# Optimization experiments

Hardware: AMD Instinct MI355X
Metric: run time of the kernel (lower is better)

Reference implementation:

```python
import jax, jax.numpy as jnp
import numpy as np

TOKEN_NUM = 81   # init default token_num
KNN_K = 2        # hardcoded in apply_clustering
LAYER_INDEX = 3


def setup_inputs() -> dict:
    key = jax.random.key(0)
    k1, k2, k3 = jax.random.split(key, 3)
    B, F, N, C = 8, 1024, 17, 512
    x = jax.random.normal(k1, (B, F, N, C), dtype=jnp.float32)
    # nn.Parameter init normal_(std=0.02)
    pos_embed_token = 0.02 * jax.random.normal(k2, (1, TOKEN_NUM, C), dtype=jnp.float32)
    # deterministic stand-in for torch.rand tie-breaker noise on density
    density_noise = jax.random.uniform(k3, (B, F), dtype=jnp.float32)
    return {"x": x, "pos_embed_token": pos_embed_token,
            "density_noise": density_noise, "current_layer": LAYER_INDEX}


def _dpc_knn_index(x_knn, density_noise, cluster_num, k):
    # x_knn: (B, F, C) pooled features; returns sorted cluster-center indices (B, cluster_num)
    B, F, C = x_knn.shape
    sq = jnp.sum(x_knn * x_knn, axis=-1)                       # (B, F)
    d2 = sq[:, :, None] + sq[:, None, :] - 2.0 * jnp.einsum('bic,bjc->bij', x_knn, x_knn)
    dist = jnp.sqrt(jnp.maximum(d2, 0.0)) / jnp.sqrt(jnp.asarray(C, x_knn.dtype))  # cdist / C**0.5
    # k smallest distances (self included, dist 0)
    neg_nearest, _ = jax.lax.top_k(-dist, k)                   # (B, F, k)
    dist_nearest = -neg_nearest
    density = jnp.exp(-jnp.mean(dist_nearest ** 2, axis=-1))   # (B, F)
    density = density + density_noise * 1e-6                   # tie-breaker
    # mask[b,i,j] = density[b,j] > density[b,i]
    mask = (density[:, None, :] > density[:, :, None]).astype(x_knn.dtype)
    dist_max = jnp.max(dist.reshape(B, -1), axis=-1)[:, None, None]
    min_dist = jnp.min(dist * mask + dist_max * (1.0 - mask), axis=-1)  # (B, F)
    score = min_dist * density
    _, index_down = jax.lax.top_k(score, cluster_num)          # (B, cluster_num)
    return jnp.sort(index_down, axis=-1)


def reference(x, pos_embed_token, density_noise, current_layer):
    # forward path only hits clustering when current_layer == layer_index
    if current_layer != LAYER_INDEX:
        return x
    B, F, N, C = x.shape
    # AdaptiveAvgPool1d(1) over joint axis after 'b f n c -> b (f c) n' == mean over n
    x_knn = jnp.mean(x, axis=2)                                # (B, F, C)
    index = _dpc_knn_index(x_knn, density_noise, TOKEN_NUM, KNN_K)
    index = jax.lax.stop_gradient(index)                       # clustering is under no_grad
    # gather selected frames: x[batch, index] -> (B, token_num, N, C)
    compressed = jnp.take_along_axis(x, index[:, :, None, None], axis=1)
    # '+ pos_embed_token' applied per (b n) f c  ==  broadcast over joints
    compressed = compressed + pos_embed_token[:, :, None, :]
    return compressed
```

## Files before the change

kernel.cpp:

```cpp
#include <hip/hip_runtime.h>
#include <math.h>
#include <float.h>

#define BB 8
#define FF 1024
#define NJ 17
#define CH 512
#define TOK 81
#define RCP_SQRT_C 0.04419417382415922f
#define LP 133

typedef short bf16x8 __attribute__((ext_vector_type(8)));
typedef float f32x16 __attribute__((ext_vector_type(16)));

static __device__ inline unsigned short f2bf(float f) {
    __bf16 h = (__bf16)f;
    return __builtin_bit_cast(unsigned short, h);
}
static __device__ inline float bf2f(unsigned short u) {
    return (float)__builtin_bit_cast(__bf16, u);
}


__global__ __launch_bounds__(256) void pool_kernel(const float* __restrict__ x,
                                                   uint4* __restrict__ fhi,
                                                   uint4* __restrict__ flo,
                                                   float* __restrict__ sq) {
    const int t = threadIdx.x;
    const int wid = t >> 6, lane = t & 63;
    const int row0 = blockIdx.x * 4;
    const int row = row0 + wid;
    const int b = row >> 10, f0 = row0 & 1023;
    const float* px = x + (size_t)row * NJ * CH + lane * 8;
    float a[8] = {};
    #pragma unroll
    for (int n = 0; n < NJ; ++n) {
        const float4 v0 = *(const float4*)(px + (size_t)n * CH);
        const float4 v1 = *(const float4*)(px + (size_t)n * CH + 4);
        a[0] += v0.x; a[1] += v0.y; a[2] += v0.z; a[3] += v0.w;
        a[4] += v1.x; a[5] += v1.y; a[6] += v1.z; a[7] += v1.w;
    }
    float ssq = 0.f;
    unsigned short hi[8], lo[8];
    #pragma unroll
    for (int j = 0; j < 8; ++j) {
        const float m = a[j] / 17.0f;
        ssq += m * m;
        hi[j] = f2bf(m);
        lo[j] = f2bf(m - bf2f(hi[j]));
    }
    #pragma unroll
    for (int off = 32; off > 0; off >>= 1) ssq += __shfl_down(ssq, off);
    if (lane == 0) sq[row] = ssq;

    uint4 uh, ul;
    uh.x = (unsigned)hi[0] | ((unsigned)hi[1] << 16);
    uh.y = (unsigned)hi[2] | ((unsigned)hi[3] << 16);
    uh.z = (unsigned)hi[4] | ((unsigned)hi[5] << 16);
    uh.w = (unsigned)hi[6] | ((unsigned)hi[7] << 16);
    ul.x = (unsigned)lo[0] | ((unsigned)lo[1] << 16);
    ul.y = (unsigned)lo[2] | ((unsigned)lo[3] << 16);
    ul.z = (unsigned)lo[4] | ((unsigned)lo[5] << 16);
    ul.w = (unsigned)lo[6] | ((unsigned)lo[7] << 16);
    __shared__ uint4 sh_hi[256], sh_lo[256];
    sh_hi[lane * 4 + wid] = uh;
    sh_lo[lane * 4 + wid] = ul;
    __syncthreads();
    const int k8 = t >> 2, fpr = t & 3;
    const int s = k8 >> 1, h = k8 & 1;
    const size_t o = (((size_t)b * 32 + s) * 2 + h) * 1024 + f0 + fpr;
    fhi[o] = sh_hi[t];
    flo[o] = sh_lo[t];
}

__global__ __launch_bounds__(256) void dist_kernel(const uint4* __restrict__ fhi,
                                                   const uint4* __restrict__ flo,
                                                   const float* __restrict__ sq,
                                                   float* __restrict__ dist) {
    int tri = blockIdx.x, rt = 0;
    while (tri >= 8 - rt) { tri -= 8 - rt; ++rt; }
    const int ct = rt + tri;
    const bool diag = (rt == ct);
    const int b = blockIdx.z;
    const int tid = threadIdx.x;
    const int w = tid >> 6, lane = tid & 63;
    const int R = rt * 128 + (w & 1) * 64;
    const int C = ct * 128 + (w >> 1) * 64;
    const int h = lane >> 5, fr = lane & 31;

    size_t a0 = ((size_t)b * 64 + h) * 1024 + R + fr;
    size_t b0 = ((size_t)b * 64 + h) * 1024 + C + fr;

    f32x16 acc00, acc01, acc10, acc11;
    #pragma unroll
    for (int i = 0; i < 16; ++i) { acc00[i] = 0.f; acc01[i] = 0.f; acc10[i] = 0.f; acc11[i] = 0.f; }

    bf16x8 A0h = *(const bf16x8*)(fhi + a0), A1h = *(const bf16x8*)(fhi + a0 + 32);
    bf16x8 A0l = *(const bf16x8*)(flo + a0), A1l = *(const bf16x8*)(flo + a0 + 32);
    bf16x8 B0h = *(const bf16x8*)(fhi + b0), B1h = *(const bf16x8*)(fhi + b0 + 32);
    bf16x8 B0l = *(const bf16x8*)(flo + b0), B1l = *(const bf16x8*)(flo + b0 + 32);

    #pragma unroll 4
    for (int s = 0; s < 32; ++s) {
        const bf16x8 cA0h = A0h, cA1h = A1h, cA0l = A0l, cA1l = A1l;
        const bf16x8 cB0h = B0h, cB1h = B1h, cB0l = B0l, cB1l = B1l;
        if (s < 31) {
            a0 += 2048; b0 += 2048;
            A0h = *(const bf16x8*)(fhi + a0); A1h = *(const bf16x8*)(fhi + a0 + 32);
            A0l = *(const bf16x8*)(flo + a0); A1l = *(const bf16x8*)(flo + a0 + 32);
            B0h = *(const bf16x8*)(fhi + b0); B1h = *(const bf16x8*)(fhi + b0 + 32);
            B0l = *(const bf16x8*)(flo + b0); B1l = *(const bf16x8*)(flo + b0 + 32);
        }
        acc00 = __builtin_amdgcn_mfma_f32_32x32x16_bf16(cA0h, cB0h, acc00, 0, 0, 0);
        acc01 = __builtin_amdgcn_mfma_f32_32x32x16_bf16(cA0h, cB1h, acc01, 0, 0, 0);
        acc10 = __builtin_amdgcn_mfma_f32_32x32x16_bf16(cA1h, cB0h, acc10, 0, 0, 0);
        acc11 = __builtin_amdgcn_mfma_f32_32x32x16_bf16(cA1h, cB1h, acc11, 0, 0, 0);
        acc00 = __builtin_amdgcn_mfma_f32_32x32x16_bf16(cA0h, cB0l, acc00, 0, 0, 0);
        acc01 = __builtin_amdgcn_mfma_f32_32x32x16_bf16(cA0h, cB1l, acc01, 0, 0, 0);
        acc10 = __builtin_amdgcn_mfma_f32_32x32x16_bf16(cA1h, cB0l, acc10, 0, 0, 0);
        acc11 = __builtin_amdgcn_mfma_f32_32x32x16_bf16(cA1h, cB1l, acc11, 0, 0, 0);
        acc00 = __builtin_amdgcn_mfma_f32_32x32x16_bf16(cA0l, cB0h, acc00, 0, 0, 0);
        acc01 = __builtin_amdgcn_mfma_f32_32x32x16_bf16(cA0l, cB1h, acc01, 0, 0, 0);
        acc10 = __builtin_amdgcn_mfma_f32_32x32x16_bf16(cA1l, cB0h, acc10, 0, 0, 0);
        acc11 = __builtin_amdgcn_mfma_f32_32x32x16_bf16(cA1l, cB1h, acc11, 0, 0, 0);
    }

    __shared__ float lds[64 * LP];
    const int bF = b * FF;
    const int R0 = rt * 128, C0 = ct * 128;
    const float sqc0 = sq[bF + C + fr], sqc1 = sq[bF + C + fr + 32];
    const int lcb = (w >> 1) * 64 + fr;

    #pragma unroll
    for (int p = 0; p < 2; ++p) {
        if ((w & 1) == p) {
            #pragma unroll
            for (int reg = 0; reg < 16; ++reg) {
                const int rp = 4 * h + (reg & 3) + 8 * (reg >> 2);
                const float sqr0 = sq[bF + R + rp];
                const float sqr1 = sq[bF + R + rp + 32];
                lds[rp * LP + lcb] =
                    sqrtf(fmaxf(sqr0 + sqc0 - 2.0f * acc00[reg], 0.f)) * RCP_SQRT_C;
                lds[rp * LP + lcb + 32] =
                    sqrtf(fmaxf(sqr0 + sqc1 - 2.0f * acc01[reg], 0.f)) * RCP_SQRT_C;
                lds[(rp + 32) * LP + lcb] =
                    sqrtf(fmaxf(sqr1 + sqc0 - 2.0f * acc10[reg], 0.f)) * RCP_SQRT_C;
                lds[(rp + 32) * LP + lcb + 32] =
                    sqrtf(fmaxf(sqr1 + sqc1 - 2.0f * acc11[reg], 0.f)) * RCP_SQRT_C;
            }
        }
        __syncthreads();
        if (!diag) {
            for (int q = tid; q < 64 * 128; q += 256) {
                const int lr = q >> 7, c = q & 127;
                dist[((size_t)bF + R0 + p * 64 + lr) * FF + C0 + c] = lds[lr * LP + c];
            }
            for (int q = tid; q < 64 * 128; q += 256) {
                const int lr = q & 63, c = q >> 6;
                dist[((size_t)bF + C0 + c) * FF + R0 + p * 64 + lr] = lds[lr * LP + c];
            }
        } else if (p == 0) {
            for (int q = tid; q < 64 * 128; q += 256) {
                const int i = q >> 7, j = q & 127;
                const float v = (i == j) ? 0.f : (i < j ? lds[i * LP + j] : lds[j * LP + i]);
                dist[((size_t)bF + R0 + i) * FF + C0 + j] = v;
            }
            for (int q = tid; q < 64 * 64; q += 256) {
                const int i = 64 + (q >> 6), j = q & 63;
                dist[((size_t)bF + R0 + i) * FF + C0 + j] = lds[j * LP + i];
            }
        } else {
            for (int q = tid; q < 64 * 64; q += 256) {
                const int i = 64 + (q >> 6), j = 64 + (q & 63);
                const float v = (i == j) ? 0.f
                               : (i < j ? lds[(i - 64) * LP + j] : lds[(j - 64) * LP + i]);
                dist[((size_t)bF + R0 + i) * FF + C0 + j] = v;
            }
        }
        __syncthreads();
    }
}

__device__ inline void merge2(float& lo0, float& lo1, float c0, float c1) {
    float n0 = fminf(lo0, c0);
    float n1 = fminf(fmaxf(lo0, c0), fminf(lo1, c1));
    lo0 = n0; lo1 = n1;
}

__global__ __launch_bounds__(256) void rowstat_kernel(const float* __restrict__ dist,
                                                      const float* __restrict__ noise,
                                                      float* __restrict__ density,
                                                      float* __restrict__ rowmax) {
    const int r = blockIdx.x * 4 + (threadIdx.x >> 6);
    const int lane = threadIdx.x & 63;
    const float* dr = dist + (size_t)r * FF;
    float lo0 = FLT_MAX, lo1 = FLT_MAX, mx = -FLT_MAX;
    #pragma unroll
    for (int j = 0; j < FF / 64; ++j) {
        const float d = dr[lane + j * 64];
        mx = fmaxf(mx, d);
        merge2(lo0, lo1, d, FLT_MAX);
    }
    #pragma unroll
    for (int off = 32; off > 0; off >>= 1) {
        const float o0 = __shfl_down(lo0, off);
        const float o1 = __shfl_down(lo1, off);
        const float om = __shfl_down(mx, off);
        merge2(lo0, lo1, o0, o1);
        mx = fmaxf(mx, om);
    }
    if (lane == 0) {
        density[r] = expf(-0.5f * (lo0 * lo0 + lo1 * lo1)) + noise[r] * 1e-6f;
        rowmax[r] = mx;
    }
}

__global__ __launch_bounds__(256) void batchmax_kernel(const float* __restrict__ rowmax,
                                                       float* __restrict__ distmax) {
    const int b = blockIdx.x, t = threadIdx.x;
    float mx = -FLT_MAX;
    for (int j = t; j < FF; j += 256) mx = fmaxf(mx, rowmax[b * FF + j]);
    #pragma unroll
    for (int off = 32; off > 0; off >>= 1) mx = fmaxf(mx, __shfl_down(mx, off));
    __shared__ float w[4];
    if ((t & 63) == 0) w[t >> 6] = mx;
    __syncthreads();
    if (t == 0) distmax[b] = fmaxf(fmaxf(w[0], w[1]), fmaxf(w[2], w[3]));
}

__global__ __launch_bounds__(256) void scoremin_kernel(const float* __restrict__ dist,
                                                       const float* __restrict__ density,
                                                       const float* __restrict__ distmax,
                                                       float* __restrict__ score) {
    const int r = blockIdx.x * 4 + (threadIdx.x >> 6);
    const int lane = threadIdx.x & 63;
    const int b = r >> 10;
    const float* dr = dist + (size_t)r * FF;
    const float* db = density + (size_t)b * FF;
    const float dme = density[r];
    float mn = FLT_MAX;
    #pragma unroll
    for (int j = 0; j < FF / 64; ++j) {
        const int c = lane + j * 64;
        if (db[c] > dme) mn = fminf(mn, dr[c]);
    }
    #pragma unroll
    for (int off = 32; off > 0; off >>= 1) mn = fminf(mn, __shfl_down(mn, off));
    if (lane == 0) {
        if (mn == FLT_MAX) mn = distmax[b];
        score[r] = mn * dme;
    }
}

__global__ __launch_bounds__(64) void topk_kernel(const float* __restrict__ score,
                                                  int* __restrict__ selsort) {
    const int b = blockIdx.x, lane = threadIdx.x;
    float s[16];
    const float* sb = score + b * FF;
    #pragma unroll
    for (int j = 0; j < 16; ++j) s[j] = sb[lane * 16 + j];
    __shared__ int sel[TOK];
    for (int it = 0; it < TOK; ++it) {
        float best = -FLT_MAX; int bi = 0;
        #pragma unroll
        for (int j = 0; j < 16; ++j) {
            if (s[j] > best) { best = s[j]; bi = lane * 16 + j; }
        }
        #pragma unroll
        for (int off = 1; off < 64; off <<= 1) {
            float ob = __shfl_xor(best, off);
            int oi = __shfl_xor(bi, off);
            if (ob > best || (ob == best && oi < bi)) { best = ob; bi = oi; }
        }
        if ((bi >> 4) == lane) s[bi & 15] = -FLT_MAX;
        if (lane == 0) sel[it] = bi;
    }
    __syncthreads();
    for (int t = lane; t < TOK; t += 64) {
        const int v = sel[t];
        int rank = 0;
        for (int j = 0; j < TOK; ++j) rank += (sel[j] < v);
        selsort[b * TOK + rank] = v;
    }
}

__global__ __launch_bounds__(256) void gather_kernel(const float* __restrict__ x,
                                                     const float* __restrict__ pos,
                                                     const int* __restrict__ selsort,
                                                     float* __restrict__ out) {
    const size_t i = (size_t)blockIdx.x * 256 + threadIdx.x;
    const size_t total = (size_t)BB * TOK * NJ * (CH / 4);
    if (i >= total) return;
    const int c4 = (int)(i & (CH / 4 - 1));
    size_t r = i >> 7;
    const int n = (int)(r % NJ); r /= NJ;
    const int t = (int)(r % TOK);
    const int b = (int)(r / TOK);
    const int f = selsort[b * TOK + t];
    float4 v = *(const float4*)(x + (((size_t)(b * FF + f)) * NJ + n) * CH + c4 * 4);
    const float4 p = *(const float4*)(pos + (size_t)t * CH + c4 * 4);
    v.x += p.x; v.y += p.y; v.z += p.z; v.w += p.w;
    *(float4*)(out + i * 4) = v;
}

extern "C" void kernel_launch(void* const* d_in, const int* in_sizes, int n_in,
                              void* d_out, int out_size, void* d_ws, size_t ws_size,
                              hipStream_t stream) {
    const float* x     = (const float*)d_in[0];
    const float* pos   = (const float*)d_in[1];
    const float* noise = (const float*)d_in[2];
    float* out = (float*)d_out;

    uint4* fhi    = (uint4*)d_ws;
    uint4* flo    = fhi + (size_t)BB * 32 * 2 * 1024;
    float* dist   = (float*)(flo + (size_t)BB * 32 * 2 * 1024);
    float* sq     = dist + (size_t)BB * FF * FF;
    float* density = sq + BB * FF;
    float* rowmax  = density + BB * FF;
    float* distmax = rowmax + BB * FF;
    float* score   = distmax + 8;
    int*   selsort = (int*)(score + BB * FF);

    pool_kernel<<<(BB * FF) / 4, 256, 0, stream>>>(x, fhi, flo, sq);
    dim3 g(36, 1, BB);
    dist_kernel<<<g, 256, 0, stream>>>(fhi, flo, sq, dist);
    rowstat_kernel<<<(BB * FF) / 4, 256, 0, stream>>>(dist, noise, density, rowmax);
    batchmax_kernel<<<BB, 256, 0, stream>>>(rowmax, distmax);
    scoremin_kernel<<<(BB * FF) / 4, 256, 0, stream>>>(dist, density, distmax, score);
    topk_kernel<<<BB, 64, 0, stream>>>(score, selsort);
    const int gtot = (int)(((size_t)BB * TOK * NJ * (CH / 4) + 255) / 256);
    gather_kernel<<<gtot, 256, 0, stream>>>(x, pos, selsort, out);
}
```

Before: 528.0 us.

## Fold batch max into rowstat via atomics and use radix-select top-k

Removes the separate batchmax kernel by having each rowstat block atomically max its partial into a per-batch slot that pool_kernel zeroes. This works because the distances are non-negative, so their float bit patterns order the same way as unsigned integers. Replaces the 81-iteration serial argmax top-k with a 4-pass byte-radix select that finds the threshold score. It then places the selected indices in sorted order directly using ballot and prefix counts. This saves one launch and cuts a long serial single-wave loop, but adds atomic contention and more intricate tie handling.

After: 488.3 us. -7.5%, faster.

```diff
diff --git a/kernel.cpp b/kernel.cpp
--- a/kernel.cpp
+++ b/kernel.cpp
@@ -25,8 +25,10 @@
 __global__ __launch_bounds__(256) void pool_kernel(const float* __restrict__ x,
                                                    uint4* __restrict__ fhi,
                                                    uint4* __restrict__ flo,
-                                                   float* __restrict__ sq) {
+                                                   float* __restrict__ sq,
+                                                   unsigned* __restrict__ dmx) {
     const int t = threadIdx.x;
+    if (blockIdx.x == 0 && t < BB) dmx[t] = 0u;
     const int wid = t >> 6, lane = t & 63;
     const int row0 = blockIdx.x * 4;
     const int row = row0 + wid;
@@ -190,8 +192,9 @@
 __global__ __launch_bounds__(256) void rowstat_kernel(const float* __restrict__ dist,
                                                       const float* __restrict__ noise,
                                                       float* __restrict__ density,
-                                                      float* __restrict__ rowmax) {
-    const int r = blockIdx.x * 4 + (threadIdx.x >> 6);
+                                                      unsigned* __restrict__ dmx) {
+    const int wid = threadIdx.x >> 6;
+    const int r = blockIdx.x * 4 + wid;
     const int lane = threadIdx.x & 63;
     const float* dr = dist + (size_t)r * FF;
     float lo0 = FLT_MAX, lo1 = FLT_MAX, mx = -FLT_MAX;
@@ -209,23 +212,16 @@
         merge2(lo0, lo1, o0, o1);
         mx = fmaxf(mx, om);
     }
+    __shared__ float wmx[4];
     if (lane == 0) {
         density[r] = expf(-0.5f * (lo0 * lo0 + lo1 * lo1)) + noise[r] * 1e-6f;
-        rowmax[r] = mx;
-    }
-}
-
-__global__ __launch_bounds__(256) void batchmax_kernel(const float* __restrict__ rowmax,
-                                                       float* __restrict__ distmax) {
-    const int b = blockIdx.x, t = threadIdx.x;
-    float mx = -FLT_MAX;
-    for (int j = t; j < FF; j += 256) mx = fmaxf(mx, rowmax[b * FF + j]);
-    #pragma unroll
-    for (int off = 32; off > 0; off >>= 1) mx = fmaxf(mx, __shfl_down(mx, off));
-    __shared__ float w[4];
-    if ((t & 63) == 0) w[t >> 6] = mx;
+        wmx[wid] = mx;
+    }
     __syncthreads();
-    if (t == 0) distmax[b] = fmaxf(fmaxf(w[0], w[1]), fmaxf(w[2], w[3]));
+    if (threadIdx.x == 0) {
+        const float m = fmaxf(fmaxf(wmx[0], wmx[1]), fmaxf(wmx[2], wmx[3]));
+        atomicMax(&dmx[blockIdx.x >> 8], __float_as_uint(m));
+    }
 }
 
 __global__ __launch_bounds__(256) void scoremin_kernel(const float* __restrict__ dist,
@@ -252,35 +248,81 @@
     }
 }
 
-__global__ __launch_bounds__(64) void topk_kernel(const float* __restrict__ score,
-                                                  int* __restrict__ selsort) {
-    const int b = blockIdx.x, lane = threadIdx.x;
-    float s[16];
+__global__ __launch_bounds__(256) void topk_kernel(const float* __restrict__ score,
+                                                   int* __restrict__ selsort) {
+    const int b = blockIdx.x, t = threadIdx.x;
+    const int w = t >> 6, lane = t & 63;
     const float* sb = score + b * FF;
-    #pragma unroll
-    for (int j = 0; j < 16; ++j) s[j] = sb[lane * 16 + j];
-    __shared__ int sel[TOK];
-    for (int it = 0; it < TOK; ++it) {
-        float best = -FLT_MAX; int bi = 0;
+    unsigned v[4];
+    #pragma unroll
+    for (int j = 0; j < 4; ++j) v[j] = __float_as_uint(sb[t + 256 * j]);
+
+    __shared__ unsigned hist[256];
+    __shared__ unsigned wtot[4];
+    __shared__ unsigned sh_byte, sh_kk;
+    unsigned prefix = 0, kk = TOK;
+    #pragma unroll
+    for (int pass = 0; pass < 4; ++pass) {
+        const int sh = 24 - 8 * pass;
+        const unsigned pmask = (pass == 0) ? 0u : (0xFFFFFFFFu << (sh + 8));
+        hist[t] = 0;
+        __syncthreads();
         #pragma unroll
-        for (int j = 0; j < 16; ++j) {
-            if (s[j] > best) { best = s[j]; bi = lane * 16 + j; }
-        }
+        for (int j = 0; j < 4; ++j)
+            if ((v[j] & pmask) == prefix) atomicAdd(&hist[(v[j] >> sh) & 255], 1u);
+        __syncthreads();
+        const unsigned cnt = hist[t];
+        unsigned s = cnt;
         #pragma unroll
         for (int off = 1; off < 64; off <<= 1) {
-            float ob = __shfl_xor(best, off);
-            int oi = __shfl_xor(bi, off);
-            if (ob > best || (ob == best && oi < bi)) { best = ob; bi = oi; }
-        }
-        if ((bi >> 4) == lane) s[bi & 15] = -FLT_MAX;
-        if (lane == 0) sel[it] = bi;
+            const unsigned o = __shfl_down(s, off);
+            if (lane + off < 64) s += o;
+        }
+        if (lane == 0) wtot[w] = s;
+        __syncthreads();
+        unsigned hi2 = 0;
+        for (int w2 = w + 1; w2 < 4; ++w2) hi2 += wtot[w2];
+        const unsigned S_incl = s + hi2;
+        const unsigned S_excl = S_incl - cnt;
+        if (S_excl < kk && kk <= S_incl) { sh_byte = (unsigned)t; sh_kk = kk - S_excl; }
+        __syncthreads();
+        prefix |= (sh_byte << sh);
+        kk = sh_kk;
+    }
+    const unsigned T = prefix;
+
+    __shared__ unsigned cgt[16], ceq[16];
+    unsigned long long bgt[4], beq[4];
+    #pragma unroll
+    for (int j = 0; j < 4; ++j) {
+        bgt[j] = __ballot(v[j] > T);
+        beq[j] = __ballot(v[j] == T);
+        if (lane == 0) {
+            cgt[j * 4 + w] = (unsigned)__popcll(bgt[j]);
+            ceq[j * 4 + w] = (unsigned)__popcll(beq[j]);
+        }
     }
     __syncthreads();
-    for (int t = lane; t < TOK; t += 64) {
-        const int v = sel[t];
-        int rank = 0;
-        for (int j = 0; j < TOK; ++j) rank += (sel[j] < v);
-        selsort[b * TOK + rank] = v;
+    const unsigned long long below = (1ULL << lane) - 1ULL;
+    #pragma unroll
+    for (int j = 0; j < 4; ++j) {
+        const bool gt = v[j] > T, eq = v[j] == T;
+        if (!gt && !eq) continue;
+        const int c = j * 4 + w;
+        unsigned bq_gt = 0, bq_eq = 0;
+        for (int cc = 0; cc < c; ++cc) { bq_gt += cgt[cc]; bq_eq += ceq[cc]; }
+        const unsigned wgt = (unsigned)__popcll(bgt[j] & below);
+        const unsigned weq = (unsigned)__popcll(beq[j] & below);
+        unsigned pos;
+        if (gt) {
+            const unsigned eq_before = bq_eq + weq;
+            pos = bq_gt + wgt + ((eq_before < kk) ? eq_before : kk);
+        } else {
+            const unsigned e = bq_eq + weq;
+            if (e >= kk) continue;
+            pos = bq_gt + wgt + e;
+        }
+        selsort[b * TOK + pos] = (int)(t + 256 * j);
     }
 }
 
@@ -316,18 +358,16 @@
     float* dist   = (float*)(flo + (size_t)BB * 32 * 2 * 1024);
     float* sq     = dist + (size_t)BB * FF * FF;
     float* density = sq + BB * FF;
-    float* rowmax  = density + BB * FF;
-    float* distmax = rowmax + BB * FF;
+    float* distmax = density + BB * FF;
     float* score   = distmax + 8;
     int*   selsort = (int*)(score + BB * FF);
 
-    pool_kernel<<<(BB * FF) / 4, 256, 0, stream>>>(x, fhi, flo, sq);
+    pool_kernel<<<(BB * FF) / 4, 256, 0, stream>>>(x, fhi, flo, sq, (unsigned*)distmax);
     dim3 g(36, 1, BB);
     dist_kernel<<<g, 256, 0, stream>>>(fhi, flo, sq, dist);
-    rowstat_kernel<<<(BB * FF) / 4, 256, 0, stream>>>(dist, noise, density, rowmax);
-    batchmax_kernel<<<BB, 256, 0, stream>>>(rowmax, distmax);
+    rowstat_kernel<<<(BB * FF) / 4, 256, 0, stream>>>(dist, noise, density, (unsigned*)distmax);
     scoremin_kernel<<<(BB * FF) / 4, 256, 0, stream>>>(dist, density, distmax, score);
-    topk_kernel<<<BB, 64, 0, stream>>>(score, selsort);
+    topk_kernel<<<BB, 256, 0, stream>>>(score, selsort);
     const int gtot = (int)(((size_t)BB * TOK * NJ * (CH / 4) + 255) / 256);
     gather_kernel<<<gtot, 256, 0, stream>>>(x, pos, selsort, out);
 }
```
